# Performance work log

Hardware: AMD Instinct MI355X
Metric: run time of the kernel (lower is better)

## Reference

```python
import jax, jax.numpy as jnp
import numpy as np

# Config (matches init_kwargs)
L, K, N = 2048, 64, 8
CB, AB, G2 = 64, 8, 9
CSB, ASB, G3 = 16, 16, 3
ROUT_ITER = 3
B = 32
LN = L // N  # 256


def squash(s):
    sq = jnp.sum(s * s, axis=-1, keepdims=True)
    return sq / (1.0 + sq) * (s / jnp.sqrt(sq + 1e-8))


def conv1d(x, w, b, pad):
    # x: [B, Cin, L], w: [Cout, Cin, k]
    y = jax.lax.conv_general_dilated(x, w, window_strides=(1,), padding=[(pad, pad)],
                                     dimension_numbers=("NCH", "OIH", "NCH"))
    return y + b[None, :, None]


def routing(V, n_iters):
    # V: [B, Ln, n, cSB, aSB]
    b_logits = jnp.zeros(V.shape[:-1], dtype=V.dtype)
    v = None
    for r in range(n_iters):
        c = jax.nn.softmax(b_logits, axis=-1)[..., None]  # [B,Ln,n,cSB,1]
        s = jnp.sum(c * V, axis=-3)                        # [B,Ln,cSB,aSB]
        v = squash(s)
        if r < n_iters - 1:
            a = jnp.sum(V * v[..., None, :, :], axis=-1)   # [B,Ln,n,cSB]
            b_logits = b_logits + jax.lax.stop_gradient(a)
    return v


def setup_inputs() -> dict:
    key = jax.random.key(0)
    ks = jax.random.split(key, 7)
    x = jax.random.normal(ks[0], (B, K, L), dtype=jnp.float32)
    w0 = jax.random.normal(ks[1], (CB, K, 1), dtype=jnp.float32) * 0.05
    b0 = jnp.zeros((CB,), dtype=jnp.float32)
    w1 = jax.random.normal(ks[2], (CB * AB, CB, G2), dtype=jnp.float32) * 0.05
    b1 = jnp.zeros((CB * AB,), dtype=jnp.float32)
    w2 = jax.random.normal(ks[3], (CSB * ASB, 1, G3, CB * AB), dtype=jnp.float32) * 0.05
    b2 = jnp.zeros((CSB * ASB,), dtype=jnp.float32)
    return {"x": x, "w0": w0, "b0": b0, "w1": w1, "b1": b1, "w2": w2, "b2": b2}


def reference(x, w0, b0, w1, b1, w2, b2):
    # convLayer: 1x1 conv1d  [B,K,L] -> [B,CB,L]
    h = conv1d(x, w0, b0, pad=0)
    # conv1: 'same' padding, odd kernel G2 -> symmetric pad G2//2
    h = conv1d(h, w1, b1, pad=G2 // 2)  # [B, CB*AB, L]
    # -> [B, Ln, n, CB*AB], squash primary capsules
    h = jnp.transpose(h, (0, 2, 1)).reshape(B, LN, N, CB * AB)
    h = squash(h)
    # -> [B, 1, Ln, n*CB*AB]
    h = h.reshape(B, LN, N * CB * AB)[:, None, :, :]
    # conv2: kernel (G3, CB*AB), stride (1, CB*AB), pad (G3//2, 0)
    pad_h = int(G3 / 2 - 0.5)
    h = jax.lax.conv_general_dilated(h, w2, window_strides=(1, CB * AB),
                                     padding=[(pad_h, pad_h), (0, 0)],
                                     dimension_numbers=("NCHW", "OIHW", "NCHW"))
    h = h + b2[None, :, None, None]                  # [B, CSB*ASB, Ln, n]
    V = jnp.transpose(h, (0, 2, 3, 1)).reshape(B, LN, N, CSB, ASB)
    v = routing(V, ROUT_ITER)                        # [B, Ln, CSB, ASB]
    return v.reshape(B, LN * CSB, ASB)
```

## Files before the change

### kernel.cpp

```cpp
#include <hip/hip_runtime.h>


#define LL    2048
#define NCAP  8
#define CO1   512
#define CO2   256
#define LNN   256

typedef __attribute__((ext_vector_type(8))) short bhalf8;
typedef __attribute__((ext_vector_type(4))) float facc4;

#define MFMA16(a, b, c) __builtin_amdgcn_mfma_f32_16x16x32_bf16(a, b, c, 0, 0, 0)

__device__ inline unsigned short f2bf(float f) {
  unsigned u = __float_as_uint(f);
  return (unsigned short)((u + 0x7FFFu + ((u >> 16) & 1u)) >> 16);
}

#if __has_builtin(__builtin_amdgcn_global_load_lds)
#define HAVE_GLDS 1
#else
#define HAVE_GLDS 0
#endif

__device__ __forceinline__ void g2l16(const unsigned short* g, unsigned short* l,
                                      int lane) {
#if HAVE_GLDS
  __builtin_amdgcn_global_load_lds(
      (const __attribute__((address_space(1))) void*)(g + lane * 8),
      (__attribute__((address_space(3))) void*)l, 16, 0, 0);
#else
  *(bhalf8*)(l + lane * 8) = *(const bhalf8*)(g + lane * 8);
#endif
}

#define OFF_W1TB 0u
#define OFF_W2P  589824u
#define OFF_H0T  1474560u
#define OFF_H1   9863168u
#define OFF_H1SQ 144080896u

__global__ __launch_bounds__(256) void prep_kernel(
    const float* __restrict__ w1, const float* __restrict__ w2,
    unsigned short* __restrict__ w1tb, unsigned short* __restrict__ w2p) {
  int idx = blockIdx.x * 256 + threadIdx.x;
  if (idx < 294912) {
    int cb = idx & 63;
    int co = (idx >> 6) & 511;
    int g  = idx >> 15;
    w1tb[idx] = f2bf(w1[(co * 64 + cb) * 9 + g]);
  } else {
    int j = idx - 294912;
    int ci = j & 63;
    int t  = j >> 6;
    int o  = t & 255;
    t >>= 8;
    int g  = t % 3;
    int cc = t / 3;
    w2p[((cc * 3 + g) * 256 + o) * 72 + ci] =
        f2bf(w2[(o * 3 + g) * 512 + cc * 64 + ci]);
  }
}

__global__ __launch_bounds__(256) void conv0_kernel(
    const float* __restrict__ x, const float* __restrict__ w0,
    const float* __restrict__ b0, unsigned short* __restrict__ h0t) {
  __shared__ __align__(16) float xt[64][128];
  __shared__ __align__(16) float w0t[64][68];
  int tid = threadIdx.x;
  int b = blockIdx.y;
  int l0 = blockIdx.x * 128;
  const float* xb = x + (size_t)b * 64 * LL;
#pragma unroll
  for (int i = 0; i < 8; i++) {
    int idx = i * 256 + tid;
    int k = idx >> 5, l4 = idx & 31;
    float4 v = *(const float4*)&xb[k * LL + l0 + l4 * 4];
    *(float4*)&xt[k][l4 * 4] = v;
  }
#pragma unroll
  for (int i = 0; i < 16; i++) {
    int idx = i * 256 + tid;
    int cb = idx >> 6, k = idx & 63;
    w0t[k][cb] = w0[idx];
  }
  __syncthreads();
  int lc = tid & 31, rc = tid >> 5;
  float acc[8][4] = {};
  for (int k = 0; k < 64; k++) {
    float4 bv = *(const float4*)&xt[k][lc * 4];
    float4 a0 = *(const float4*)&w0t[k][rc * 8];
    float4 a1 = *(const float4*)&w0t[k][rc * 8 + 4];
    float a[8] = {a0.x, a0.y, a0.z, a0.w, a1.x, a1.y, a1.z, a1.w};
    float bb4[4] = {bv.x, bv.y, bv.z, bv.w};
#pragma unroll
    for (int i = 0; i < 8; i++)
#pragma unroll
      for (int j = 0; j < 4; j++) acc[i][j] += a[i] * bb4[j];
  }
  float bias[8];
#pragma unroll
  for (int i = 0; i < 8; i++) bias[i] = b0[rc * 8 + i];
#pragma unroll
  for (int j = 0; j < 4; j++) {
    bhalf8 o;
#pragma unroll
    for (int i = 0; i < 8; i++) o[i] = (short)f2bf(acc[i][j] + bias[i]);
    *(bhalf8*)&h0t[((size_t)b * LL + l0 + lc * 4 + j) * 64 + rc * 8] = o;
  }
}

__global__ __launch_bounds__(512) void conv1_mfma(
    const unsigned short* __restrict__ h0t, const unsigned short* __restrict__ w1tb,
    const float* __restrict__ b1, float* __restrict__ h1) {
  __shared__ __align__(16) unsigned short Xt[136 * 72];
  __shared__ __align__(16) unsigned short Wg[256 * 72];
  int tid = threadIdx.x;
  int b = blockIdx.z;
  int co0 = blockIdx.y * 256;
  int l0 = blockIdx.x * 128;
#pragma unroll
  for (int it = 0; it < 3; it++) {
    int idx = it * 512 + tid;
    if (idx < 1088) {
      int row = idx >> 3, c8 = (idx & 7) * 8;
      int l = l0 - 4 + row;
      bhalf8 v = (bhalf8)0;
      if (l >= 0 && l < LL) v = *(const bhalf8*)&h0t[((size_t)b * LL + l) * 64 + c8];
      *(bhalf8*)&Xt[row * 72 + c8] = v;
    }
  }
  int wid = tid >> 6, lane = tid & 63;
  int wr = wid >> 1, wc = wid & 1;
  int r16 = lane & 15, k8 = lane >> 4;
  facc4 acc[4][4] = {};
  for (int g = 0; g < 9; g++) {
    __syncthreads();
#pragma unroll
    for (int it = 0; it < 4; it++) {
      int idx = it * 512 + tid;
      int row = idx >> 3, c8 = (idx & 7) * 8;
      *(bhalf8*)&Wg[row * 72 + c8] =
          *(const bhalf8*)&w1tb[((size_t)(g * 512 + co0 + row)) * 64 + c8];
    }
    __syncthreads();
#pragma unroll
    for (int ks = 0; ks < 2; ks++) {
      bhalf8 A[4], Bf[4];
#pragma unroll
      for (int mi = 0; mi < 4; mi++)
        A[mi] = *(const bhalf8*)&Wg[(wr * 64 + mi * 16 + r16) * 72 + ks * 32 + k8 * 8];
#pragma unroll
      for (int ni = 0; ni < 4; ni++)
        Bf[ni] = *(const bhalf8*)&Xt[(wc * 64 + ni * 16 + r16 + g) * 72 + ks * 32 + k8 * 8];
#pragma unroll
      for (int mi = 0; mi < 4; mi++)
#pragma unroll
        for (int ni = 0; ni < 4; ni++)
          acc[mi][ni] = MFMA16(A[mi], Bf[ni], acc[mi][ni]);
    }
  }
#pragma unroll
  for (int mi = 0; mi < 4; mi++) {
    int co_w = co0 + wr * 64 + mi * 16 + k8 * 4;
    float4 bias = *(const float4*)&b1[co_w];
#pragma unroll
    for (int ni = 0; ni < 4; ni++) {
      int l_w = l0 + wc * 64 + ni * 16 + r16;
      float* p = &h1[((size_t)b * LL + l_w) * CO1 + co_w];
      *(float4*)p = make_float4(acc[mi][ni][0] + bias.x, acc[mi][ni][1] + bias.y,
                                acc[mi][ni][2] + bias.z, acc[mi][ni][3] + bias.w);
    }
  }
}

__global__ __launch_bounds__(256) void squash1_kernel(
    const float* __restrict__ h1, unsigned short* __restrict__ h1sq) {
  int tid = threadIdx.x;
  int wave = tid >> 6, lane = tid & 63;
  size_t row = (size_t)blockIdx.x * 4 + wave;
  const float* p = h1 + row * CO1;
  float4 v0 = *(const float4*)(p + lane * 8);
  float4 v1 = *(const float4*)(p + lane * 8 + 4);
  float sq = v0.x * v0.x + v0.y * v0.y + v0.z * v0.z + v0.w * v0.w +
             v1.x * v1.x + v1.y * v1.y + v1.z * v1.z + v1.w * v1.w;
#pragma unroll
  for (int m = 1; m < 64; m <<= 1) sq += __shfl_xor(sq, m, 64);
  float s = sq / (1.f + sq) / sqrtf(sq + 1e-8f);
  bhalf8 o;
  o[0] = (short)f2bf(v0.x * s); o[1] = (short)f2bf(v0.y * s);
  o[2] = (short)f2bf(v0.z * s); o[3] = (short)f2bf(v0.w * s);
  o[4] = (short)f2bf(v1.x * s); o[5] = (short)f2bf(v1.y * s);
  o[6] = (short)f2bf(v1.z * s); o[7] = (short)f2bf(v1.w * s);
  int b = (int)(row >> 11), l = (int)(row & 2047);
  int ln = l >> 3, n = l & 7;
  int cc = lane >> 3, ci8 = (lane & 7) * 8;
  *(bhalf8*)&h1sq[((size_t)(((b * 8 + n) * 8 + cc) * 256 + ln)) * 72 + ci8] = o;
}

__global__ __launch_bounds__(512, 2) void conv2_mfma(
    const unsigned short* __restrict__ h1sq, const unsigned short* __restrict__ w2p,
    const float* __restrict__ b2, float* __restrict__ V) {
  __shared__ __align__(16) unsigned short Hc[258 * 72];
  __shared__ __align__(16) unsigned short Wl[3 * 256 * 72];
  int tid = threadIdx.x;
  int bn = blockIdx.x;
  int b = bn >> 3, n = bn & 7;
  int wid = tid >> 6, lane = tid & 63;
  int wr = wid >> 2, wc = wid & 3;
  int r16 = lane & 15, k8 = lane >> 4;
  facc4 acc[8][4] = {};
  for (int cc = 0; cc < 8; cc++) {
    __syncthreads();
    if (tid < 72) { Hc[tid] = 0; Hc[257 * 72 + tid] = 0; }
    const unsigned short* hsrc = h1sq + (size_t)((b * 8 + n) * 8 + cc) * (256 * 72);
    for (int ch = wid; ch < 36; ch += 8)
      g2l16(hsrc + ch * 512, &Hc[72 + ch * 512], lane);
    const unsigned short* wsrc = w2p + (size_t)cc * (3 * 256 * 72);
    for (int ch = wid; ch < 108; ch += 8)
      g2l16(wsrc + ch * 512, &Wl[ch * 512], lane);
    __syncthreads();
    for (int g = 0; g < 3; g++) {
#pragma unroll
      for (int ks = 0; ks < 2; ks++) {
        bhalf8 Bv[4];
#pragma unroll
        for (int ni = 0; ni < 4; ni++)
          Bv[ni] = *(const bhalf8*)&Hc[(wc * 64 + ni * 16 + r16 + g) * 72 + ks * 32 + k8 * 8];
#pragma unroll
        for (int mi = 0; mi < 8; mi++) {
          bhalf8 Av = *(const bhalf8*)&Wl[(g * 256 + wr * 128 + mi * 16 + r16) * 72 + ks * 32 + k8 * 8];
#pragma unroll
          for (int ni = 0; ni < 4; ni++)
            acc[mi][ni] = MFMA16(Av, Bv[ni], acc[mi][ni]);
        }
      }
    }
  }
#pragma unroll
  for (int mi = 0; mi < 8; mi++) {
    int o_w = wr * 128 + mi * 16 + k8 * 4;
    float4 bias = *(const float4*)&b2[o_w];
#pragma unroll
    for (int ni = 0; ni < 4; ni++) {
      int ln_w = wc * 64 + ni * 16 + r16;
      float* p = &V[(((size_t)b * LNN + ln_w) * NCAP + n) * CO2 + o_w];
      *(float4*)p = make_float4(acc[mi][ni][0] + bias.x, acc[mi][ni][1] + bias.y,
                                acc[mi][ni][2] + bias.z, acc[mi][ni][3] + bias.w);
    }
  }
}

__global__ __launch_bounds__(256) void routing_kernel(
    const float* __restrict__ V, float* __restrict__ out) {
  __shared__ float Vs[8][16][17];
  __shared__ float blog[8][16];
  __shared__ float cbuf[8][16];
  __shared__ float vbuf[16][17];
  int tid = threadIdx.x;
  size_t base = (size_t)blockIdx.x * 2048;
#pragma unroll
  for (int i = 0; i < 8; i++) {
    int idx = i * 256 + tid;
    int nn = idx >> 8, r = idx & 255;
    Vs[nn][r >> 4][r & 15] = V[base + idx];
  }
  if (tid < 128) blog[tid >> 4][tid & 15] = 0.f;
  __syncthreads();
  int csb = tid >> 4, asb = tid & 15;
  for (int r = 0; r < 3; r++) {
    if (tid < 128) {
      int nn = tid >> 4, cs = tid & 15;
      float xv = blog[nn][cs];
      float m = xv;
#pragma unroll
      for (int d = 1; d < 16; d <<= 1) m = fmaxf(m, __shfl_xor(m, d, 16));
      float e = expf(xv - m);
      float ssum = e;
#pragma unroll
      for (int d = 1; d < 16; d <<= 1) ssum += __shfl_xor(ssum, d, 16);
      cbuf[nn][cs] = e / ssum;
    }
    __syncthreads();
    float s = 0.f;
#pragma unroll
    for (int q = 0; q < 8; q++) s += cbuf[q][csb] * Vs[q][csb][asb];
    float sq = s * s;
#pragma unroll
    for (int d = 1; d < 16; d <<= 1) sq += __shfl_xor(sq, d, 16);
    float vv = s * (sq / (1.f + sq) / sqrtf(sq + 1e-8f));
    if (r < 2) {
      vbuf[csb][asb] = vv;
      __syncthreads();
      if (tid < 128) {
        int nn = tid >> 4, cs = tid & 15;
        float a = 0.f;
#pragma unroll
        for (int q = 0; q < 16; q++) a += Vs[nn][cs][q] * vbuf[cs][q];
        blog[nn][cs] += a;
      }
      __syncthreads();
    } else {
      out[(size_t)blockIdx.x * 256 + tid] = vv;
    }
  }
}

extern "C" void kernel_launch(void* const* d_in, const int* in_sizes, int n_in,
                              void* d_out, int out_size, void* d_ws, size_t ws_size,
                              hipStream_t stream) {
  const float* x  = (const float*)d_in[0];
  const float* w0 = (const float*)d_in[1];
  const float* b0 = (const float*)d_in[2];
  const float* w1 = (const float*)d_in[3];
  const float* b1 = (const float*)d_in[4];
  const float* w2 = (const float*)d_in[5];
  const float* b2 = (const float*)d_in[6];
  float* out = (float*)d_out;
  char* ws = (char*)d_ws;
  unsigned short* w1tb = (unsigned short*)(ws + OFF_W1TB);
  unsigned short* w2p  = (unsigned short*)(ws + OFF_W2P);
  unsigned short* h0t  = (unsigned short*)(ws + OFF_H0T);
  float*          h1   = (float*)(ws + OFF_H1);
  unsigned short* h1sq = (unsigned short*)(ws + OFF_H1SQ);
  float*          Vb   = (float*)(ws + OFF_H1);

  prep_kernel<<<2688, 256, 0, stream>>>(w1, w2, w1tb, w2p);
  conv0_kernel<<<dim3(16, 32), 256, 0, stream>>>(x, w0, b0, h0t);
  conv1_mfma<<<dim3(16, 2, 32), 512, 0, stream>>>(h0t, w1tb, b1, h1);
  squash1_kernel<<<16384, 256, 0, stream>>>(h1, h1sq);
  conv2_mfma<<<256, 512, 0, stream>>>(h1sq, w2p, b2, Vb);
  routing_kernel<<<8192, 256, 0, stream>>>(Vb, out);
}
```

Measured before the change: 263.9 us.

## Read conv weights directly from global memory and swizzle conv2 activation tile in LDS

Conv1 and conv2 no longer stage weight tiles in LDS. Each wave loads its MFMA A-fragments straight from global memory, which relies on L2/L1 reuse across blocks and removes two barriers per filter tap in conv1. The squashed activation buffer becomes a plain [b,n,ln,512] layout without the 72-element padding, and conv2 loads it into an unpadded LDS tile using an XOR swizzle to avoid bank conflicts. This frees enough LDS to raise occupancy, but exposes global-load latency in the inner MFMA loops.

```diff
diff --git a/kernel.cpp b/kernel.cpp
--- a/kernel.cpp
+++ b/kernel.cpp
@@ -23,14 +23,14 @@
 #define HAVE_GLDS 0
 #endif
 
-__device__ __forceinline__ void g2l16(const unsigned short* g, unsigned short* l,
-                                      int lane) {
+__device__ __forceinline__ void g2l_lane(const unsigned short* g_lane,
+                                         unsigned short* l_base, int lane) {
 #if HAVE_GLDS
   __builtin_amdgcn_global_load_lds(
-      (const __attribute__((address_space(1))) void*)(g + lane * 8),
-      (__attribute__((address_space(3))) void*)l, 16, 0, 0);
+      (const __attribute__((address_space(1))) void*)g_lane,
+      (__attribute__((address_space(3))) void*)l_base, 16, 0, 0);
 #else
-  *(bhalf8*)(l + lane * 8) = *(const bhalf8*)(g + lane * 8);
+  *(bhalf8*)(l_base + lane * 8) = *(const bhalf8*)g_lane;
 #endif
 }
 
@@ -57,7 +57,7 @@
     t >>= 8;
     int g  = t % 3;
     int cc = t / 3;
-    w2p[((cc * 3 + g) * 256 + o) * 72 + ci] =
+    w2p[((cc * 3 + g) * 256 + o) * 64 + ci] =
         f2bf(w2[(o * 3 + g) * 512 + cc * 64 + ci]);
   }
 }
@@ -114,7 +114,6 @@
     const unsigned short* __restrict__ h0t, const unsigned short* __restrict__ w1tb,
     const float* __restrict__ b1, float* __restrict__ h1) {
   __shared__ __align__(16) unsigned short Xt[136 * 72];
-  __shared__ __align__(16) unsigned short Wg[256 * 72];
   int tid = threadIdx.x;
   int b = blockIdx.z;
   int co0 = blockIdx.y * 256;
@@ -130,26 +129,19 @@
       *(bhalf8*)&Xt[row * 72 + c8] = v;
     }
   }
+  __syncthreads();
   int wid = tid >> 6, lane = tid & 63;
   int wr = wid >> 1, wc = wid & 1;
   int r16 = lane & 15, k8 = lane >> 4;
   facc4 acc[4][4] = {};
   for (int g = 0; g < 9; g++) {
-    __syncthreads();
-#pragma unroll
-    for (int it = 0; it < 4; it++) {
-      int idx = it * 512 + tid;
-      int row = idx >> 3, c8 = (idx & 7) * 8;
-      *(bhalf8*)&Wg[row * 72 + c8] =
-          *(const bhalf8*)&w1tb[((size_t)(g * 512 + co0 + row)) * 64 + c8];
-    }
-    __syncthreads();
 #pragma unroll
     for (int ks = 0; ks < 2; ks++) {
       bhalf8 A[4], Bf[4];
 #pragma unroll
       for (int mi = 0; mi < 4; mi++)
-        A[mi] = *(const bhalf8*)&Wg[(wr * 64 + mi * 16 + r16) * 72 + ks * 32 + k8 * 8];
+        A[mi] = *(const bhalf8*)&w1tb[((size_t)(g * 512 + co0 + wr * 64 + mi * 16 + r16)) * 64 +
+                                      ks * 32 + k8 * 8];
 #pragma unroll
       for (int ni = 0; ni < 4; ni++)
         Bf[ni] = *(const bhalf8*)&Xt[(wc * 64 + ni * 16 + r16 + g) * 72 + ks * 32 + k8 * 8];
@@ -194,46 +186,57 @@
   o[6] = (short)f2bf(v1.z * s); o[7] = (short)f2bf(v1.w * s);
   int b = (int)(row >> 11), l = (int)(row & 2047);
   int ln = l >> 3, n = l & 7;
-  int cc = lane >> 3, ci8 = (lane & 7) * 8;
-  *(bhalf8*)&h1sq[((size_t)(((b * 8 + n) * 8 + cc) * 256 + ln)) * 72 + ci8] = o;
-}
-
-__global__ __launch_bounds__(512, 2) void conv2_mfma(
+  *(bhalf8*)&h1sq[((size_t)((b * 8 + n) * 256 + ln)) * 512 + lane * 8] = o;
+}
+
+__global__ __launch_bounds__(512) void conv2_mfma(
     const unsigned short* __restrict__ h1sq, const unsigned short* __restrict__ w2p,
     const float* __restrict__ b2, float* __restrict__ V) {
-  __shared__ __align__(16) unsigned short Hc[258 * 72];
-  __shared__ __align__(16) unsigned short Wl[3 * 256 * 72];
+  __shared__ __align__(16) unsigned short Hc[258 * 64];
   int tid = threadIdx.x;
   int bn = blockIdx.x;
   int b = bn >> 3, n = bn & 7;
   int wid = tid >> 6, lane = tid & 63;
   int wr = wid >> 2, wc = wid & 3;
   int r16 = lane & 15, k8 = lane >> 4;
+  int row8 = lane >> 3, slot = lane & 7;
   facc4 acc[8][4] = {};
+  const unsigned short* hbase = h1sq + (size_t)(b * 8 + n) * 256 * 512;
   for (int cc = 0; cc < 8; cc++) {
     __syncthreads();
-    if (tid < 72) { Hc[tid] = 0; Hc[257 * 72 + tid] = 0; }
-    const unsigned short* hsrc = h1sq + (size_t)((b * 8 + n) * 8 + cc) * (256 * 72);
-    for (int ch = wid; ch < 36; ch += 8)
-      g2l16(hsrc + ch * 512, &Hc[72 + ch * 512], lane);
-    const unsigned short* wsrc = w2p + (size_t)cc * (3 * 256 * 72);
-    for (int ch = wid; ch < 108; ch += 8)
-      g2l16(wsrc + ch * 512, &Wl[ch * 512], lane);
+    if (tid < 128) {
+      int r = tid >> 6, c = tid & 63;
+      Hc[(r ? 257 : 0) * 64 + c] = 0;
+    }
+    for (int ch = wid; ch < 32; ch += 8) {
+      int r = 1 + ch * 8 + row8;
+      int gslot = slot ^ (r & 7);
+      g2l_lane(&hbase[(size_t)(r - 1) * 512 + cc * 64 + gslot * 8],
+               &Hc[(1 + ch * 8) * 64], lane);
+    }
     __syncthreads();
+    const unsigned short* wbase = w2p + (size_t)cc * (3 * 256 * 64);
+#pragma unroll
     for (int g = 0; g < 3; g++) {
 #pragma unroll
       for (int ks = 0; ks < 2; ks++) {
+        bhalf8 Av[8];
+#pragma unroll
+        for (int mi = 0; mi < 8; mi++)
+          Av[mi] = *(const bhalf8*)&wbase[(size_t)(g * 256 + wr * 128 + mi * 16 + r16) * 64 +
+                                          ks * 32 + k8 * 8];
         bhalf8 Bv[4];
 #pragma unroll
-        for (int ni = 0; ni < 4; ni++)
-          Bv[ni] = *(const bhalf8*)&Hc[(wc * 64 + ni * 16 + r16 + g) * 72 + ks * 32 + k8 * 8];
-#pragma unroll
-        for (int mi = 0; mi < 8; mi++) {
-          bhalf8 Av = *(const bhalf8*)&Wl[(g * 256 + wr * 128 + mi * 16 + r16) * 72 + ks * 32 + k8 * 8];
+        for (int ni = 0; ni < 4; ni++) {
+          int rr = wc * 64 + ni * 16 + r16 + g;
+          int sl = (ks * 4 + k8) ^ (rr & 7);
+          Bv[ni] = *(const bhalf8*)&Hc[rr * 64 + sl * 8];
+        }
+#pragma unroll
+        for (int mi = 0; mi < 8; mi++)
 #pragma unroll
           for (int ni = 0; ni < 4; ni++)
-            acc[mi][ni] = MFMA16(Av, Bv[ni], acc[mi][ni]);
-        }
+            acc[mi][ni] = MFMA16(Av[mi], Bv[ni], acc[mi][ni]);
       }
     }
   }
```

Measured after the change: 332.3 us. 1.26x slower.
